# Performance work log

Measured on AMD Instinct MI355X. Metric: run time of the kernel, lower is better.

## Reference

```python
import jax, jax.numpy as jnp
import numpy as np
from jax import lax

EPS = 1e-4
THRESHOLD = 0.0


@jax.custom_vjp
def ternary(x):
    return jnp.where(x <= -THRESHOLD, -1.0,
                     jnp.where(x >= THRESHOLD, 1.0, 0.0)).astype(x.dtype)


def _ternary_fwd(x):
    return ternary(x), x


def _ternary_bwd(x, g):
    # STE: pass gradient where -1 < x < 1, zero where |x| >= 1
    mask = (x < 1.0) & (x > -1.0)
    return (g * mask.astype(g.dtype),)


ternary.defvjp(_ternary_fwd, _ternary_bwd)


def setup_inputs() -> dict:
    key = jax.random.key(0)
    k1, k2, k3 = jax.random.split(key, 3)
    N, C_in, H, W = 32, 256, 56, 56
    C_out, K = 256, 3
    x = jax.random.normal(k1, (N, C_in, H, W), dtype=jnp.float32)
    gamma = jnp.ones((C_in,), dtype=jnp.float32)
    beta = jnp.zeros((C_in,), dtype=jnp.float32)
    fan_in = C_in * K * K
    weight = jax.random.normal(k2, (C_out, C_in, K, K), dtype=jnp.float32) / np.sqrt(fan_in)
    bias = jax.random.normal(k3, (C_out,), dtype=jnp.float32) * 0.01
    return {"x": x, "gamma": gamma, "beta": beta, "weight": weight, "bias": bias}


def reference(x, gamma, beta, weight, bias):
    # BatchNorm2d (training mode: batch statistics, biased var), eps=1e-4
    mean = jnp.mean(x, axis=(0, 2, 3), keepdims=True)
    var = jnp.mean(jnp.square(x - mean), axis=(0, 2, 3), keepdims=True)
    xn = (x - mean) * lax.rsqrt(var + EPS)
    xn = xn * gamma[None, :, None, None] + beta[None, :, None, None]
    # Ternarize to {-1, 0, 1}
    t = ternary(xn)
    # Conv2d stride=1, padding=1 (NCHW / OIHW)
    y = lax.conv_general_dilated(
        t, weight, window_strides=(1, 1), padding=[(1, 1), (1, 1)],
        dimension_numbers=("NCHW", "OIHW", "NCHW"))
    y = y + bias[None, :, None, None]
    return jax.nn.relu(y)
```

## Files before the change

kernel.cpp:

```cpp
#include <hip/hip_runtime.h>
#include <stdint.h>

#define NN 32
#define CI 256
#define CO 256
#define HH 56
#define WW 56
#define TPH 58
#define TPW 72
#define CNT (NN*HH*WW)

typedef int i32x4 __attribute__((ext_vector_type(4)));

__device__ __forceinline__ void gld16(const void* g, void* l) {
    __builtin_amdgcn_global_load_lds(
        (const __attribute__((address_space(1))) void*)(uintptr_t)g,
        (__attribute__((address_space(3))) void*)(uint32_t)(uintptr_t)l,
        16, 0, 0);
}

__global__ void stats_part(const float* __restrict__ x, double* __restrict__ part) {
    const int c = blockIdx.x, sp = blockIdx.y;
    double s = 0.0, ss = 0.0;
    const size_t base = ((size_t)(sp * 4) * CI + c) * 3136;
    for (int idx = threadIdx.x; idx < 4 * 784; idx += 256) {
        int nl = idx / 784, q = idx % 784;
        const float4 v = *(const float4*)(x + base + (size_t)nl * CI * 3136 + q * 4);
        double a = v.x, b = v.y, cc = v.z, d = v.w;
        s  += (a + b) + (cc + d);
        ss += (a * a + b * b) + (cc * cc + d * d);
    }
    for (int off = 32; off > 0; off >>= 1) {
        s  += __shfl_down(s, off, 64);
        ss += __shfl_down(ss, off, 64);
    }
    __shared__ double red[8];
    int wid = threadIdx.x >> 6, lane = threadIdx.x & 63;
    if (lane == 0) { red[wid] = s; red[4 + wid] = ss; }
    __syncthreads();
    if (threadIdx.x == 0) {
        part[(sp * 256 + c) * 2]     = (red[0] + red[1]) + (red[2] + red[3]);
        part[(sp * 256 + c) * 2 + 1] = (red[4] + red[5]) + (red[6] + red[7]);
    }
}

__global__ void wtrans_kernel(const float* __restrict__ w,
                              int8_t* __restrict__ wT,
                              float* __restrict__ qscale) {
    const int co = blockIdx.x;
    const float* wp = w + (size_t)co * 2304;
    float v[9], m = 0.f;
#pragma unroll
    for (int it = 0; it < 9; ++it) {
        v[it] = wp[threadIdx.x + it * 256];
        m = fmaxf(m, fabsf(v[it]));
    }
    for (int off = 32; off > 0; off >>= 1) m = fmaxf(m, __shfl_down(m, off, 64));
    __shared__ float red[4];
    __shared__ float qsh;
    int wid = threadIdx.x >> 6, lane = threadIdx.x & 63;
    if (lane == 0) red[wid] = m;
    __syncthreads();
    if (threadIdx.x == 0) {
        float mx = fmaxf(fmaxf(red[0], red[1]), fmaxf(red[2], red[3]));
        float q = (mx > 0.f) ? mx / 127.f : 1.f;
        qsh = q;
        qscale[co] = q;
    }
    __syncthreads();
    const float q = qsh;
#pragma unroll
    for (int it = 0; it < 9; ++it) {
        int idx = threadIdx.x + it * 256;
        int ci = idx / 9, tap = idx % 9;
        int chunk = ci >> 6, cis = ci & 63;
        int iq = __float2int_rn(v[it] / q);
        iq = iq > 127 ? 127 : (iq < -127 ? -127 : iq);
        wT[((size_t)(tap * 4 + chunk) * 256 + co) * 64 + cis] = (int8_t)iq;
    }
}

__global__ void ternarize_kernel(const float* __restrict__ x,
                                 const double* __restrict__ part,
                                 const float* __restrict__ gamma,
                                 const float* __restrict__ beta,
                                 int8_t* __restrict__ tp) {
    const int h = blockIdx.x, n = blockIdx.y;
    i32x4* rowp = (i32x4*)(tp + ((size_t)n * TPH + h) * TPW * CI);
    if (h == 0 || h == TPH - 1) {
        const i32x4 z = {0, 0, 0, 0};
        for (int p = threadIdx.x; p < TPW * 16; p += 256) rowp[p] = z;
        return;
    }
    __shared__ double Ssc[256], Ssh[256];
    {
        const int c = threadIdx.x;
        double S = 0.0, SS = 0.0;
#pragma unroll
        for (int sp = 0; sp < 8; ++sp) {
            S  += part[(sp * 256 + c) * 2];
            SS += part[(sp * 256 + c) * 2 + 1];
        }
        double mean = S / (double)CNT;
        double var  = SS / (double)CNT - mean * mean;
        double invstd = 1.0 / sqrt(var + 1e-4);
        double scale = (double)gamma[c] * invstd;
        Ssc[c] = scale;
        Ssh[c] = (double)beta[c] - mean * scale;
    }
    __shared__ int8_t L[56 * 260];
    __syncthreads();
    const int hin = h - 1;
    const size_t xb = ((size_t)n * CI) * 3136 + (size_t)hin * 56;
    for (int idx = threadIdx.x; idx < CI * 14; idx += 256) {
        int ci = idx / 14, w4 = idx - ci * 14;
        const float4 v = *(const float4*)(x + xb + (size_t)ci * 3136 + w4 * 4);
        const double sc = Ssc[ci], sh = Ssh[ci];
        const int w = w4 * 4;
        L[(w + 0) * 260 + ci] = (fma(sc, (double)v.x, sh) > 0.0) ? (int8_t)1 : (int8_t)-1;
        L[(w + 1) * 260 + ci] = (fma(sc, (double)v.y, sh) > 0.0) ? (int8_t)1 : (int8_t)-1;
        L[(w + 2) * 260 + ci] = (fma(sc, (double)v.z, sh) > 0.0) ? (int8_t)1 : (int8_t)-1;
        L[(w + 3) * 260 + ci] = (fma(sc, (double)v.w, sh) > 0.0) ? (int8_t)1 : (int8_t)-1;
    }
    __syncthreads();
    for (int p = threadIdx.x; p < TPW * 16; p += 256) {
        int wo = p >> 4, c16 = p & 15;
        i32x4 v = {0, 0, 0, 0};
        if (wo >= 1 && wo <= 56) {
            const int* lp = (const int*)&L[(wo - 1) * 260 + c16 * 16];
            v.x = lp[0]; v.y = lp[1]; v.z = lp[2]; v.w = lp[3];
        }
        rowp[p] = v;
    }
}

#define CONV_LDS (6 * 4 * TPW * 16)

__device__ __forceinline__ void stage6(const int8_t* __restrict__ g0,
                                       int8_t* lbuf, int chunk, int tid) {
#pragma unroll
    for (int j = 0; j < 7; ++j) {
        int p = tid + j * 256;
        if (j < 6 || tid < 192) {
            int row = p / 288, rem = p - row * 288;
            int s = rem / 72, wp = rem - s * 72;
            gld16(g0 + (size_t)row * TPW * CI + wp * 256 + chunk * 64 + s * 16,
                  lbuf + p * 16);
        }
    }
}

__launch_bounds__(256, 2)
__global__ void conv_kernel(const int8_t* __restrict__ wT,
                            const int8_t* __restrict__ tp,
                            const float* __restrict__ bias,
                            const float* __restrict__ qscale,
                            float* __restrict__ out) {
    const int bid  = blockIdx.x;
    const int lin  = (bid & 7) * 112 + (bid >> 3);
    const int co_t = lin & 1;
    const int yb   = (lin >> 1) % 14;
    const int n    = lin / 28;
    const int h0   = yb * 4;

    const int tid  = threadIdx.x;
    const int lane = tid & 63, wid = tid >> 6;
    const int l15 = lane & 15, qd = lane >> 4;
    const int m_off = (wid & 1) * 64;
    const int rs = (wid >> 1) * 2;
    const int aoff = l15 * 64 + qd * 16;

    __shared__ __align__(16) int8_t Bsh[2 * CONV_LDS];

    i32x4 acc[4][4][2];
#pragma unroll
    for (int i = 0; i < 4; ++i)
#pragma unroll
        for (int j = 0; j < 4; ++j)
#pragma unroll
            for (int r = 0; r < 2; ++r) acc[i][j][r] = (i32x4){0, 0, 0, 0};

    const int8_t* g0 = tp + ((size_t)n * TPH + h0) * TPW * CI;

#define LOADA(dst, cc_, tap_) do {                                              \
    const int8_t* ap_ = wT +                                                    \
        (((size_t)((tap_) * 4 + (cc_)) * 256 + co_t * 128 + m_off) << 6) + aoff;\
    dst[0] = *(const i32x4*)(ap_);                                              \
    dst[1] = *(const i32x4*)(ap_ + 1024);                                       \
    dst[2] = *(const i32x4*)(ap_ + 2048);                                       \
    dst[3] = *(const i32x4*)(ap_ + 3072);                                       \
} while (0)

    i32x4 a[2][4];
    stage6(g0, Bsh, 0, tid);
    LOADA(a[0], 0, 0);

    for (int c2 = 0; c2 < 2; ++c2) {
#pragma unroll
        for (int cc = 0; cc < 2; ++cc) {
            const int c = c2 * 2 + cc;
            __syncthreads();
            if (c < 3) stage6(g0, Bsh + (cc ^ 1) * CONV_LDS, c + 1, tid);
            const int8_t* lb = Bsh + cc * CONV_LDS;
#pragma unroll
            for (int tap = 0; tap < 9; ++tap) {
                const int kh = tap / 3, kw = tap % 3;
                const int cur = (cc * 9 + tap) & 1, nxt = cur ^ 1;
                i32x4 b[4][2];
#pragma unroll
                for (int j = 0; j < 4; ++j) {
                    const int wp = j * 16 + l15 + kw;
#pragma unroll
                    for (int r = 0; r < 2; ++r)
                        b[j][r] = *(const i32x4*)&lb[(((rs + r + kh) * 4 + qd) * 72 + wp) * 16];
                }
                if (tap < 8)      LOADA(a[nxt], c, tap + 1);
                else if (c < 3)   LOADA(a[nxt], c + 1, 0);
                __builtin_amdgcn_s_setprio(1);
#pragma unroll
                for (int i = 0; i < 4; ++i)
#pragma unroll
                    for (int j = 0; j < 4; ++j)
#pragma unroll
                        for (int r = 0; r < 2; ++r)
                            acc[i][j][r] = __builtin_amdgcn_mfma_i32_16x16x64_i8(
                                a[cur][i], b[j][r], acc[i][j][r], 0, 0, 0);
                __builtin_amdgcn_s_setprio(0);
            }
        }
    }
#undef LOADA

    const int h_out = h0 + rs;
#pragma unroll
    for (int i = 0; i < 4; ++i) {
        const int co = co_t * 128 + m_off + i * 16 + qd * 4;
        const float4 bv = *(const float4*)&bias[co];
        const float4 qv = *(const float4*)&qscale[co];
        const float bb[4] = {bv.x, bv.y, bv.z, bv.w};
        const float qq[4] = {qv.x, qv.y, qv.z, qv.w};
#pragma unroll
        for (int j = 0; j < 4; ++j) {
            const int w = j * 16 + l15;
            if (w < 56) {
#pragma unroll
                for (int rr = 0; rr < 2; ++rr) {
                    const size_t ob = (((size_t)n * CO + co) * HH + (h_out + rr)) * WW + w;
#pragma unroll
                    for (int r = 0; r < 4; ++r) {
                        float v = (float)acc[i][j][rr][r] * qq[r] + bb[r];
                        out[ob + (size_t)r * (HH * WW)] = v > 0.f ? v : 0.f;
                    }
                }
            }
        }
    }
}

extern "C" void kernel_launch(void* const* d_in, const int* in_sizes, int n_in,
                              void* d_out, int out_size, void* d_ws, size_t ws_size,
                              hipStream_t stream) {
    const float* x      = (const float*)d_in[0];
    const float* gamma  = (const float*)d_in[1];
    const float* beta   = (const float*)d_in[2];
    const float* weight = (const float*)d_in[3];
    const float* bias   = (const float*)d_in[4];
    float* out = (float*)d_out;

    double* part    = (double*)d_ws;
    float*  qscale  = (float*) ((char*)d_ws + 36864);
    int8_t* wT      = (int8_t*)((char*)d_ws + 65536);
    int8_t* tp      = (int8_t*)((char*)d_ws + 1048576);

    wtrans_kernel<<<256, 256, 0, stream>>>(weight, wT, qscale);
    stats_part<<<dim3(256, 8), 256, 0, stream>>>(x, part);
    ternarize_kernel<<<dim3(TPH, NN), 256, 0, stream>>>(x, part, gamma, beta, tp);
    conv_kernel<<<896, 256, 0, stream>>>(wT, tp, bias, qscale, out);
}
```

Measured before the change: 328.0 us.

## Fuse ternarization into conv kernel and merge weight-prep with stats kernel

Removes the separate ternarize kernel and its padded int8 intermediate tensor: the conv kernel now loads fp32 activations directly, applies the batchnorm sign test per channel chunk in registers, and writes packed int8 tiles into LDS, overlapping the next chunk's global loads with MFMA work. Weight quantization and stats partial sums are merged into one launch to cut a kernel launch. The trade is that each conv block re-reads a fp32 halo (6 rows for 4 outputs), which is more global traffic than the int8 intermediate, and register pressure rises with the 24 float4 staging registers. Each block also zeroes its LDS buffers and recomputes the BN scale and shift.

```diff
diff --git a/kernel.cpp b/kernel.cpp
--- a/kernel.cpp
+++ b/kernel.cpp
@@ -6,153 +6,138 @@
 #define CO 256
 #define HH 56
 #define WW 56
-#define TPH 58
-#define TPW 72
 #define CNT (NN*HH*WW)
 
 typedef int i32x4 __attribute__((ext_vector_type(4)));
 
-__device__ __forceinline__ void gld16(const void* g, void* l) {
-    __builtin_amdgcn_global_load_lds(
-        (const __attribute__((address_space(1))) void*)(uintptr_t)g,
-        (__attribute__((address_space(3))) void*)(uint32_t)(uintptr_t)l,
-        16, 0, 0);
-}
-
-__global__ void stats_part(const float* __restrict__ x, double* __restrict__ part) {
-    const int c = blockIdx.x, sp = blockIdx.y;
-    double s = 0.0, ss = 0.0;
-    const size_t base = ((size_t)(sp * 4) * CI + c) * 3136;
-    for (int idx = threadIdx.x; idx < 4 * 784; idx += 256) {
-        int nl = idx / 784, q = idx % 784;
-        const float4 v = *(const float4*)(x + base + (size_t)nl * CI * 3136 + q * 4);
-        double a = v.x, b = v.y, cc = v.z, d = v.w;
-        s  += (a + b) + (cc + d);
-        ss += (a * a + b * b) + (cc * cc + d * d);
-    }
-    for (int off = 32; off > 0; off >>= 1) {
-        s  += __shfl_down(s, off, 64);
-        ss += __shfl_down(ss, off, 64);
-    }
-    __shared__ double red[8];
-    int wid = threadIdx.x >> 6, lane = threadIdx.x & 63;
-    if (lane == 0) { red[wid] = s; red[4 + wid] = ss; }
-    __syncthreads();
-    if (threadIdx.x == 0) {
-        part[(sp * 256 + c) * 2]     = (red[0] + red[1]) + (red[2] + red[3]);
-        part[(sp * 256 + c) * 2 + 1] = (red[4] + red[5]) + (red[6] + red[7]);
-    }
-}
-
-__global__ void wtrans_kernel(const float* __restrict__ w,
-                              int8_t* __restrict__ wT,
-                              float* __restrict__ qscale) {
-    const int co = blockIdx.x;
-    const float* wp = w + (size_t)co * 2304;
-    float v[9], m = 0.f;
-#pragma unroll
-    for (int it = 0; it < 9; ++it) {
-        v[it] = wp[threadIdx.x + it * 256];
-        m = fmaxf(m, fabsf(v[it]));
-    }
-    for (int off = 32; off > 0; off >>= 1) m = fmaxf(m, __shfl_down(m, off, 64));
-    __shared__ float red[4];
-    __shared__ float qsh;
-    int wid = threadIdx.x >> 6, lane = threadIdx.x & 63;
-    if (lane == 0) red[wid] = m;
-    __syncthreads();
-    if (threadIdx.x == 0) {
-        float mx = fmaxf(fmaxf(red[0], red[1]), fmaxf(red[2], red[3]));
-        float q = (mx > 0.f) ? mx / 127.f : 1.f;
-        qsh = q;
-        qscale[co] = q;
-    }
-    __syncthreads();
-    const float q = qsh;
-#pragma unroll
-    for (int it = 0; it < 9; ++it) {
-        int idx = threadIdx.x + it * 256;
-        int ci = idx / 9, tap = idx % 9;
-        int chunk = ci >> 6, cis = ci & 63;
-        int iq = __float2int_rn(v[it] / q);
-        iq = iq > 127 ? 127 : (iq < -127 ? -127 : iq);
-        wT[((size_t)(tap * 4 + chunk) * 256 + co) * 64 + cis] = (int8_t)iq;
-    }
-}
-
-__global__ void ternarize_kernel(const float* __restrict__ x,
-                                 const double* __restrict__ part,
-                                 const float* __restrict__ gamma,
-                                 const float* __restrict__ beta,
-                                 int8_t* __restrict__ tp) {
-    const int h = blockIdx.x, n = blockIdx.y;
-    i32x4* rowp = (i32x4*)(tp + ((size_t)n * TPH + h) * TPW * CI);
-    if (h == 0 || h == TPH - 1) {
-        const i32x4 z = {0, 0, 0, 0};
-        for (int p = threadIdx.x; p < TPW * 16; p += 256) rowp[p] = z;
-        return;
-    }
-    __shared__ double Ssc[256], Ssh[256];
-    {
-        const int c = threadIdx.x;
-        double S = 0.0, SS = 0.0;
-#pragma unroll
-        for (int sp = 0; sp < 8; ++sp) {
-            S  += part[(sp * 256 + c) * 2];
-            SS += part[(sp * 256 + c) * 2 + 1];
-        }
-        double mean = S / (double)CNT;
-        double var  = SS / (double)CNT - mean * mean;
-        double invstd = 1.0 / sqrt(var + 1e-4);
-        double scale = (double)gamma[c] * invstd;
-        Ssc[c] = scale;
-        Ssh[c] = (double)beta[c] - mean * scale;
-    }
-    __shared__ int8_t L[56 * 260];
-    __syncthreads();
-    const int hin = h - 1;
-    const size_t xb = ((size_t)n * CI) * 3136 + (size_t)hin * 56;
-    for (int idx = threadIdx.x; idx < CI * 14; idx += 256) {
-        int ci = idx / 14, w4 = idx - ci * 14;
-        const float4 v = *(const float4*)(x + xb + (size_t)ci * 3136 + w4 * 4);
-        const double sc = Ssc[ci], sh = Ssh[ci];
-        const int w = w4 * 4;
-        L[(w + 0) * 260 + ci] = (fma(sc, (double)v.x, sh) > 0.0) ? (int8_t)1 : (int8_t)-1;
-        L[(w + 1) * 260 + ci] = (fma(sc, (double)v.y, sh) > 0.0) ? (int8_t)1 : (int8_t)-1;
-        L[(w + 2) * 260 + ci] = (fma(sc, (double)v.z, sh) > 0.0) ? (int8_t)1 : (int8_t)-1;
-        L[(w + 3) * 260 + ci] = (fma(sc, (double)v.w, sh) > 0.0) ? (int8_t)1 : (int8_t)-1;
-    }
-    __syncthreads();
-    for (int p = threadIdx.x; p < TPW * 16; p += 256) {
-        int wo = p >> 4, c16 = p & 15;
-        i32x4 v = {0, 0, 0, 0};
-        if (wo >= 1 && wo <= 56) {
-            const int* lp = (const int*)&L[(wo - 1) * 260 + c16 * 16];
-            v.x = lp[0]; v.y = lp[1]; v.z = lp[2]; v.w = lp[3];
-        }
-        rowp[p] = v;
-    }
-}
-
-#define CONV_LDS (6 * 4 * TPW * 16)
-
-__device__ __forceinline__ void stage6(const int8_t* __restrict__ g0,
-                                       int8_t* lbuf, int chunk, int tid) {
-#pragma unroll
-    for (int j = 0; j < 7; ++j) {
-        int p = tid + j * 256;
-        if (j < 6 || tid < 192) {
-            int row = p / 288, rem = p - row * 288;
-            int s = rem / 72, wp = rem - s * 72;
-            gld16(g0 + (size_t)row * TPW * CI + wp * 256 + chunk * 64 + s * 16,
-                  lbuf + p * 16);
+__global__ void prep_kernel(const float* __restrict__ w,
+                            const float* __restrict__ x,
+                            int8_t* __restrict__ wT,
+                            float* __restrict__ qscale,
+                            double* __restrict__ part) {
+    const int bid = blockIdx.x;
+    if (bid < 256) {
+        const int co = bid;
+        const float* wp = w + (size_t)co * 2304;
+        float v[9], m = 0.f;
+#pragma unroll
+        for (int it = 0; it < 9; ++it) {
+            v[it] = wp[threadIdx.x + it * 256];
+            m = fmaxf(m, fabsf(v[it]));
+        }
+        for (int off = 32; off > 0; off >>= 1) m = fmaxf(m, __shfl_down(m, off, 64));
+        __shared__ float redf[4];
+        __shared__ float qsh;
+        int wid = threadIdx.x >> 6, lane = threadIdx.x & 63;
+        if (lane == 0) redf[wid] = m;
+        __syncthreads();
+        if (threadIdx.x == 0) {
+            float mx = fmaxf(fmaxf(redf[0], redf[1]), fmaxf(redf[2], redf[3]));
+            float q = (mx > 0.f) ? mx / 127.f : 1.f;
+            qsh = q;
+            qscale[co] = q;
+        }
+        __syncthreads();
+        const float q = qsh;
+#pragma unroll
+        for (int it = 0; it < 9; ++it) {
+            int idx = threadIdx.x + it * 256;
+            int ci = idx / 9, tap = idx % 9;
+            int chunk = ci >> 6, cis = ci & 63;
+            int iq = __float2int_rn(v[it] / q);
+            iq = iq > 127 ? 127 : (iq < -127 ? -127 : iq);
+            wT[((size_t)(tap * 4 + chunk) * 256 + co) * 64 + cis] = (int8_t)iq;
+        }
+    } else {
+        const int idx = bid - 256;
+        const int c = idx & 255, sp = idx >> 8;
+        double s = 0.0, ss = 0.0;
+        const size_t base = ((size_t)(sp * 4) * CI + c) * 3136;
+        for (int i = threadIdx.x; i < 4 * 784; i += 256) {
+            int nl = i / 784, qq = i % 784;
+            const float4 v = *(const float4*)(x + base + (size_t)nl * CI * 3136 + qq * 4);
+            double a = v.x, b = v.y, cc = v.z, d = v.w;
+            s  += (a + b) + (cc + d);
+            ss += (a * a + b * b) + (cc * cc + d * d);
+        }
+        for (int off = 32; off > 0; off >>= 1) {
+            s  += __shfl_down(s, off, 64);
+            ss += __shfl_down(ss, off, 64);
+        }
+        __shared__ double redd[8];
+        int wid = threadIdx.x >> 6, lane = threadIdx.x & 63;
+        if (lane == 0) { redd[wid] = s; redd[4 + wid] = ss; }
+        __syncthreads();
+        if (threadIdx.x == 0) {
+            part[(sp * 256 + c) * 2]     = (redd[0] + redd[1]) + (redd[2] + redd[3]);
+            part[(sp * 256 + c) * 2 + 1] = (redd[4] + redd[5]) + (redd[6] + redd[7]);
+        }
+    }
+}
+
+#define BUF_B 27776
+#define SLOT(row, s, wp) ((row) * 4624 + (s) * 1168 + (wp) * 16)
+
+__device__ __forceinline__ void loadf(const float* __restrict__ xb, int chunk,
+                                      int h0, int tid, float4 (&f)[6][4]) {
+    const float* cb = xb + (size_t)chunk * 64 * 3136;
+#pragma unroll
+    for (int k = 0; k < 6; ++k) {
+        if (k < 5 || tid < 64) {
+            int q = tid + k * 256;
+            int ci4 = q / 84, rem = q - ci4 * 84;
+            int row = rem / 14, w4 = rem - row * 14;
+            int h = h0 - 1 + row;
+            if ((unsigned)h < 56u) {
+#pragma unroll
+                for (int u = 0; u < 4; ++u)
+                    f[k][u] = *(const float4*)(cb + (size_t)(ci4 * 4 + u) * 3136 + h * 56 + w4 * 4);
+            }
+        }
+    }
+}
+
+__device__ __forceinline__ void transf(float4 (&f)[6][4],
+                                       const double* __restrict__ Ssc,
+                                       const double* __restrict__ Ssh,
+                                       int chunk, int h0, int tid,
+                                       int8_t* __restrict__ lbuf) {
+    const int cbase = chunk * 64;
+#pragma unroll
+    for (int k = 0; k < 6; ++k) {
+        if (k < 5 || tid < 64) {
+            int q = tid + k * 256;
+            int ci4 = q / 84, rem = q - ci4 * 84;
+            int row = rem / 14, w4 = rem - row * 14;
+            if ((unsigned)(h0 - 1 + row) < 56u) {
+                int words[4] = {0, 0, 0, 0};
+#pragma unroll
+                for (int u = 0; u < 4; ++u) {
+                    const double sc = Ssc[cbase + ci4 * 4 + u];
+                    const double sh = Ssh[cbase + ci4 * 4 + u];
+                    const float4 v = f[k][u];
+                    const float vv[4] = {v.x, v.y, v.z, v.w};
+#pragma unroll
+                    for (int j = 0; j < 4; ++j) {
+                        int b = (fma(sc, (double)vv[j], sh) > 0.0) ? 0x01 : 0xFF;
+                        words[j] |= b << (8 * u);
+                    }
+                }
+                const int base = SLOT(row, ci4 >> 2, 0) + (ci4 & 3) * 4;
+#pragma unroll
+                for (int j = 0; j < 4; ++j)
+                    *(int*)&lbuf[base + (w4 * 4 + 1 + j) * 16] = words[j];
+            }
         }
     }
 }
 
 __launch_bounds__(256, 2)
 __global__ void conv_kernel(const int8_t* __restrict__ wT,
-                            const int8_t* __restrict__ tp,
+                            const float* __restrict__ x,
+                            const double* __restrict__ part,
+                            const float* __restrict__ gamma,
+                            const float* __restrict__ beta,
                             const float* __restrict__ bias,
                             const float* __restrict__ qscale,
                             float* __restrict__ out) {
@@ -170,7 +155,29 @@
     const int rs = (wid >> 1) * 2;
     const int aoff = l15 * 64 + qd * 16;
 
-    __shared__ __align__(16) int8_t Bsh[2 * CONV_LDS];
+    __shared__ __align__(16) int8_t Bsh[2 * BUF_B];
+    __shared__ double Ssc[256], Ssh[256];
+
+    {
+        const int c = tid;
+        double S = 0.0, SS = 0.0;
+#pragma unroll
+        for (int sp = 0; sp < 8; ++sp) {
+            S  += part[(sp * 256 + c) * 2];
+            SS += part[(sp * 256 + c) * 2 + 1];
+        }
+        double mean = S / (double)CNT;
+        double var  = SS / (double)CNT - mean * mean;
+        double invstd = 1.0 / sqrt(var + 1e-4);
+        double scale = (double)gamma[c] * invstd;
+        Ssc[c] = scale;
+        Ssh[c] = (double)beta[c] - mean * scale;
+    }
+    {
+        i32x4 z = {0, 0, 0, 0};
+        for (int p = tid; p < 2 * BUF_B / 16; p += 256)
+            ((i32x4*)Bsh)[p] = z;
+    }
 
     i32x4 acc[4][4][2];
 #pragma unroll
@@ -180,7 +187,7 @@
 #pragma unroll
             for (int r = 0; r < 2; ++r) acc[i][j][r] = (i32x4){0, 0, 0, 0};
 
-    const int8_t* g0 = tp + ((size_t)n * TPH + h0) * TPW * CI;
+    const float* xb = x + (size_t)n * CI * 3136;
 
 #define LOADA(dst, cc_, tap_) do {                                              \
     const int8_t* ap_ = wT +                                                    \
@@ -191,8 +198,13 @@
     dst[3] = *(const i32x4*)(ap_ + 3072);                                       \
 } while (0)
 
+    float4 f[6][4];
     i32x4 a[2][4];
-    stage6(g0, Bsh, 0, tid);
+
+    loadf(xb, 0, h0, tid, f);
+    __syncthreads();
+    transf(f, Ssc, Ssh, 0, h0, tid, Bsh);
+    loadf(xb, 1, h0, tid, f);
     LOADA(a[0], 0, 0);
 
     for (int c2 = 0; c2 < 2; ++c2) {
@@ -200,8 +212,9 @@
         for (int cc = 0; cc < 2; ++cc) {
             const int c = c2 * 2 + cc;
             __syncthreads();
-            if (c < 3) stage6(g0, Bsh + (cc ^ 1) * CONV_LDS, c + 1, tid);
-            const int8_t* lb = Bsh + cc * CONV_LDS;
+            if (c < 3) transf(f, Ssc, Ssh, c + 1, h0, tid, Bsh + (cc ^ 1) * BUF_B);
+            if (c < 2) loadf(xb, c + 2, h0, tid, f);
+            const int8_t* lb = Bsh + cc * BUF_B;
 #pragma unroll
             for (int tap = 0; tap < 9; ++tap) {
                 const int kh = tap / 3, kw = tap % 3;
@@ -212,7 +225,7 @@
                     const int wp = j * 16 + l15 + kw;
 #pragma unroll
                     for (int r = 0; r < 2; ++r)
-                        b[j][r] = *(const i32x4*)&lb[(((rs + r + kh) * 4 + qd) * 72 + wp) * 16];
+                        b[j][r] = *(const i32x4*)&lb[SLOT(rs + r + kh, qd, wp)];
                 }
                 if (tap < 8)      LOADA(a[nxt], c, tap + 1);
                 else if (c < 3)   LOADA(a[nxt], c + 1, 0);
@@ -270,10 +283,7 @@
     double* part    = (double*)d_ws;
     float*  qscale  = (float*) ((char*)d_ws + 36864);
     int8_t* wT      = (int8_t*)((char*)d_ws + 65536);
-    int8_t* tp      = (int8_t*)((char*)d_ws + 1048576);
-
-    wtrans_kernel<<<256, 256, 0, stream>>>(weight, wT, qscale);
-    stats_part<<<dim3(256, 8), 256, 0, stream>>>(x, part);
-    ternarize_kernel<<<dim3(TPH, NN), 256, 0, stream>>>(x, part, gamma, beta, tp);
-    conv_kernel<<<896, 256, 0, stream>>>(wT, tp, bias, qscale, out);
-}
+
+    prep_kernel<<<2304, 256, 0, stream>>>(weight, x, wT, qscale, part);
+    conv_kernel<<<896, 256, 0, stream>>>(wT, x, part, gamma, beta, bias, qscale, out);
+}
```

Result: slower. 474.9 us (+44.8%).

## Merge prep kernels and restage conv tile as swizzled single-shot LDS load

Applied to the files above, without the earlier changes.

Fuses the weight quantisation and batch-statistics kernels into a single launch. Changes the ternarized activation layout to channel-chunk-major per row and makes each conv block compute two output rows, loading its full input tile into LDS once with an XOR-style slot swizzle instead of double-buffering per channel chunk. This is meant to cut launch overhead and LDS bank conflicts and to raise block count. In exchange it drops load/compute overlap, increases halo and weight re-reading per output, and halves accumulator state.

```diff
diff --git a/kernel.cpp b/kernel.cpp
--- a/kernel.cpp
+++ b/kernel.cpp
@@ -19,64 +19,68 @@
         16, 0, 0);
 }
 
-__global__ void stats_part(const float* __restrict__ x, double* __restrict__ part) {
-    const int c = blockIdx.x, sp = blockIdx.y;
-    double s = 0.0, ss = 0.0;
-    const size_t base = ((size_t)(sp * 4) * CI + c) * 3136;
-    for (int idx = threadIdx.x; idx < 4 * 784; idx += 256) {
-        int nl = idx / 784, q = idx % 784;
-        const float4 v = *(const float4*)(x + base + (size_t)nl * CI * 3136 + q * 4);
-        double a = v.x, b = v.y, cc = v.z, d = v.w;
-        s  += (a + b) + (cc + d);
-        ss += (a * a + b * b) + (cc * cc + d * d);
-    }
-    for (int off = 32; off > 0; off >>= 1) {
-        s  += __shfl_down(s, off, 64);
-        ss += __shfl_down(ss, off, 64);
-    }
-    __shared__ double red[8];
-    int wid = threadIdx.x >> 6, lane = threadIdx.x & 63;
-    if (lane == 0) { red[wid] = s; red[4 + wid] = ss; }
-    __syncthreads();
-    if (threadIdx.x == 0) {
-        part[(sp * 256 + c) * 2]     = (red[0] + red[1]) + (red[2] + red[3]);
-        part[(sp * 256 + c) * 2 + 1] = (red[4] + red[5]) + (red[6] + red[7]);
-    }
-}
-
-__global__ void wtrans_kernel(const float* __restrict__ w,
-                              int8_t* __restrict__ wT,
-                              float* __restrict__ qscale) {
-    const int co = blockIdx.x;
-    const float* wp = w + (size_t)co * 2304;
-    float v[9], m = 0.f;
-#pragma unroll
-    for (int it = 0; it < 9; ++it) {
-        v[it] = wp[threadIdx.x + it * 256];
-        m = fmaxf(m, fabsf(v[it]));
-    }
-    for (int off = 32; off > 0; off >>= 1) m = fmaxf(m, __shfl_down(m, off, 64));
-    __shared__ float red[4];
-    __shared__ float qsh;
-    int wid = threadIdx.x >> 6, lane = threadIdx.x & 63;
-    if (lane == 0) red[wid] = m;
-    __syncthreads();
-    if (threadIdx.x == 0) {
-        float mx = fmaxf(fmaxf(red[0], red[1]), fmaxf(red[2], red[3]));
-        float q = (mx > 0.f) ? mx / 127.f : 1.f;
-        qsh = q;
-        qscale[co] = q;
-    }
-    __syncthreads();
-    const float q = qsh;
-#pragma unroll
-    for (int it = 0; it < 9; ++it) {
-        int idx = threadIdx.x + it * 256;
-        int ci = idx / 9, tap = idx % 9;
-        int chunk = ci >> 6, cis = ci & 63;
-        int iq = __float2int_rn(v[it] / q);
-        iq = iq > 127 ? 127 : (iq < -127 ? -127 : iq);
-        wT[((size_t)(tap * 4 + chunk) * 256 + co) * 64 + cis] = (int8_t)iq;
+__global__ void prep_kernel(const float* __restrict__ w,
+                            const float* __restrict__ x,
+                            int8_t* __restrict__ wT,
+                            float* __restrict__ qscale,
+                            double* __restrict__ part) {
+    const int bid = blockIdx.x;
+    if (bid < 256) {
+        const int co = bid;
+        const float* wp = w + (size_t)co * 2304;
+        float v[9], m = 0.f;
+#pragma unroll
+        for (int it = 0; it < 9; ++it) {
+            v[it] = wp[threadIdx.x + it * 256];
+            m = fmaxf(m, fabsf(v[it]));
+        }
+        for (int off = 32; off > 0; off >>= 1) m = fmaxf(m, __shfl_down(m, off, 64));
+        __shared__ float redf[4];
+        __shared__ float qsh;
+        int wid = threadIdx.x >> 6, lane = threadIdx.x & 63;
+        if (lane == 0) redf[wid] = m;
+        __syncthreads();
+        if (threadIdx.x == 0) {
+            float mx = fmaxf(fmaxf(redf[0], redf[1]), fmaxf(redf[2], redf[3]));
+            float q = (mx > 0.f) ? mx / 127.f : 1.f;
+            qsh = q;
+            qscale[co] = q;
+        }
+        __syncthreads();
+        const float q = qsh;
+#pragma unroll
+        for (int it = 0; it < 9; ++it) {
+            int idx = threadIdx.x + it * 256;
+            int ci = idx / 9, tap = idx % 9;
+            int chunk = ci >> 6, cis = ci & 63;
+            int iq = __float2int_rn(v[it] / q);
+            iq = iq > 127 ? 127 : (iq < -127 ? -127 : iq);
+            wT[((size_t)(tap * 4 + chunk) * 256 + co) * 64 + cis] = (int8_t)iq;
+        }
+    } else {
+        const int idx = bid - 256;
+        const int c = idx & 255, sp = idx >> 8;
+        double s = 0.0, ss = 0.0;
+        const size_t base = ((size_t)(sp * 4) * CI + c) * 3136;
+        for (int i = threadIdx.x; i < 4 * 784; i += 256) {
+            int nl = i / 784, qq = i % 784;
+            const float4 v = *(const float4*)(x + base + (size_t)nl * CI * 3136 + qq * 4);
+            double a = v.x, b = v.y, cc = v.z, d = v.w;
+            s  += (a + b) + (cc + d);
+            ss += (a * a + b * b) + (cc * cc + d * d);
+        }
+        for (int off = 32; off > 0; off >>= 1) {
+            s  += __shfl_down(s, off, 64);
+            ss += __shfl_down(ss, off, 64);
+        }
+        __shared__ double redd[8];
+        int wid = threadIdx.x >> 6, lane = threadIdx.x & 63;
+        if (lane == 0) { redd[wid] = s; redd[4 + wid] = ss; }
+        __syncthreads();
+        if (threadIdx.x == 0) {
+            part[(sp * 256 + c) * 2]     = (redd[0] + redd[1]) + (redd[2] + redd[3]);
+            part[(sp * 256 + c) * 2 + 1] = (redd[4] + redd[5]) + (redd[6] + redd[7]);
+        }
     }
 }
 
@@ -130,25 +134,12 @@
             const int* lp = (const int*)&L[(wo - 1) * 260 + c16 * 16];
             v.x = lp[0]; v.y = lp[1]; v.z = lp[2]; v.w = lp[3];
         }
-        rowp[p] = v;
-    }
-}
-
-#define CONV_LDS (6 * 4 * TPW * 16)
-
-__device__ __forceinline__ void stage6(const int8_t* __restrict__ g0,
-                                       int8_t* lbuf, int chunk, int tid) {
-#pragma unroll
-    for (int j = 0; j < 7; ++j) {
-        int p = tid + j * 256;
-        if (j < 6 || tid < 192) {
-            int row = p / 288, rem = p - row * 288;
-            int s = rem / 72, wp = rem - s * 72;
-            gld16(g0 + (size_t)row * TPW * CI + wp * 256 + chunk * 64 + s * 16,
-                  lbuf + p * 16);
-        }
-    }
-}
+        const int chunk = c16 >> 2, s = c16 & 3;
+        rowp[chunk * 288 + wo * 4 + s] = v;
+    }
+}
+
+#define BUF_B (4 * 4 * TPW * 64)
 
 __launch_bounds__(256, 2)
 __global__ void conv_kernel(const int8_t* __restrict__ wT,
@@ -156,31 +147,41 @@
                             const float* __restrict__ bias,
                             const float* __restrict__ qscale,
                             float* __restrict__ out) {
-    const int bid  = blockIdx.x;
-    const int lin  = (bid & 7) * 112 + (bid >> 3);
+    const int bid = blockIdx.x;
+    const int lin = (bid & 7) * 224 + (bid >> 3);
     const int co_t = lin & 1;
-    const int yb   = (lin >> 1) % 14;
-    const int n    = lin / 28;
-    const int h0   = yb * 4;
+    const int yb   = (lin >> 1) % 28;
+    const int n    = lin / 56;
+    const int h0   = yb * 2;
 
     const int tid  = threadIdx.x;
     const int lane = tid & 63, wid = tid >> 6;
     const int l15 = lane & 15, qd = lane >> 4;
     const int m_off = (wid & 1) * 64;
-    const int rs = (wid >> 1) * 2;
+    const int rowsel = wid >> 1;
     const int aoff = l15 * 64 + qd * 16;
 
-    __shared__ __align__(16) int8_t Bsh[2 * CONV_LDS];
-
-    i32x4 acc[4][4][2];
+    __shared__ __align__(16) int8_t Bsh[BUF_B];
+
+    i32x4 acc[4][4];
 #pragma unroll
     for (int i = 0; i < 4; ++i)
 #pragma unroll
-        for (int j = 0; j < 4; ++j)
-#pragma unroll
-            for (int r = 0; r < 2; ++r) acc[i][j][r] = (i32x4){0, 0, 0, 0};
-
-    const int8_t* g0 = tp + ((size_t)n * TPH + h0) * TPW * CI;
+        for (int j = 0; j < 4; ++j) acc[i][j] = (i32x4){0, 0, 0, 0};
+
+    {
+        const int8_t* g0 = tp + ((size_t)n * TPH + h0) * TPW * CI;
+#pragma unroll
+        for (int j = 0; j < 18; ++j) {
+            int p = tid + j * 256;
+            int row = p / 1152, rem = p - row * 1152;
+            int chunk = rem / 288, rem2 = rem - chunk * 288;
+            int wp = rem2 >> 2, s = rem2 & 3;
+            int g = (s - wp) & 3;
+            gld16(g0 + (size_t)row * (TPW * CI) + chunk * (TPW * 64) + wp * 64 + g * 16,
+                  Bsh + p * 16);
+        }
+    }
 
 #define LOADA(dst, cc_, tap_) do {                                              \
     const int8_t* ap_ = wT +                                                    \
@@ -192,27 +193,24 @@
 } while (0)
 
     i32x4 a[2][4];
-    stage6(g0, Bsh, 0, tid);
     LOADA(a[0], 0, 0);
+    __syncthreads();
 
     for (int c2 = 0; c2 < 2; ++c2) {
 #pragma unroll
         for (int cc = 0; cc < 2; ++cc) {
             const int c = c2 * 2 + cc;
-            __syncthreads();
-            if (c < 3) stage6(g0, Bsh + (cc ^ 1) * CONV_LDS, c + 1, tid);
-            const int8_t* lb = Bsh + cc * CONV_LDS;
 #pragma unroll
             for (int tap = 0; tap < 9; ++tap) {
                 const int kh = tap / 3, kw = tap % 3;
                 const int cur = (cc * 9 + tap) & 1, nxt = cur ^ 1;
-                i32x4 b[4][2];
+                i32x4 b[4];
 #pragma unroll
                 for (int j = 0; j < 4; ++j) {
                     const int wp = j * 16 + l15 + kw;
-#pragma unroll
-                    for (int r = 0; r < 2; ++r)
-                        b[j][r] = *(const i32x4*)&lb[(((rs + r + kh) * 4 + qd) * 72 + wp) * 16];
+                    const int slot = (qd + wp) & 3;
+                    b[j] = *(const i32x4*)&Bsh[
+                        (((rowsel + kh) * 4 + c) * TPW + wp) * 64 + slot * 16];
                 }
                 if (tap < 8)      LOADA(a[nxt], c, tap + 1);
                 else if (c < 3)   LOADA(a[nxt], c + 1, 0);
@@ -221,17 +219,15 @@
                 for (int i = 0; i < 4; ++i)
 #pragma unroll
                     for (int j = 0; j < 4; ++j)
-#pragma unroll
-                        for (int r = 0; r < 2; ++r)
-                            acc[i][j][r] = __builtin_amdgcn_mfma_i32_16x16x64_i8(
-                                a[cur][i], b[j][r], acc[i][j][r], 0, 0, 0);
+                        acc[i][j] = __builtin_amdgcn_mfma_i32_16x16x64_i8(
+                            a[cur][i], b[j], acc[i][j], 0, 0, 0);
                 __builtin_amdgcn_s_setprio(0);
             }
         }
     }
 #undef LOADA
 
-    const int h_out = h0 + rs;
+    const int h_out = h0 + rowsel;
 #pragma unroll
     for (int i = 0; i < 4; ++i) {
         const int co = co_t * 128 + m_off + i * 16 + qd * 4;
@@ -243,14 +239,11 @@
         for (int j = 0; j < 4; ++j) {
             const int w = j * 16 + l15;
             if (w < 56) {
-#pragma unroll
-                for (int rr = 0; rr < 2; ++rr) {
-                    const size_t ob = (((size_t)n * CO + co) * HH + (h_out + rr)) * WW + w;
-#pragma unroll
-                    for (int r = 0; r < 4; ++r) {
-                        float v = (float)acc[i][j][rr][r] * qq[r] + bb[r];
-                        out[ob + (size_t)r * (HH * WW)] = v > 0.f ? v : 0.f;
-                    }
+                const size_t ob = (((size_t)n * CO + co) * HH + h_out) * WW + w;
+#pragma unroll
+                for (int r = 0; r < 4; ++r) {
+                    float v = (float)acc[i][j][r] * qq[r] + bb[r];
+                    out[ob + (size_t)r * (HH * WW)] = v > 0.f ? v : 0.f;
                 }
             }
         }
@@ -272,8 +265,7 @@
     int8_t* wT      = (int8_t*)((char*)d_ws + 65536);
     int8_t* tp      = (int8_t*)((char*)d_ws + 1048576);
 
-    wtrans_kernel<<<256, 256, 0, stream>>>(weight, wT, qscale);
-    stats_part<<<dim3(256, 8), 256, 0, stream>>>(x, part);
+    prep_kernel<<<2304, 256, 0, stream>>>(weight, x, wT, qscale, part);
     ternarize_kernel<<<dim3(TPH, NN), 256, 0, stream>>>(x, part, gamma, beta, tp);
-    conv_kernel<<<896, 256, 0, stream>>>(wT, tp, bias, qscale, out);
-}
+    conv_kernel<<<1792, 256, 0, stream>>>(wT, tp, bias, qscale, out);
+}
```

After: 289.4 us. -11.7%, faster.
